# Optimization experiments

Hardware: AMD Instinct MI355X
Metric: run time of the kernel (lower is better)

Reference implementation:

```python
import jax, jax.numpy as jnp
import numpy as np

DEP_NUM, HEAD_NUM, BSZ, DIM, REL = 96, 96, 16, 512, 128


def setup_inputs() -> dict:
    key = jax.random.key(0)
    k1, k2, k3, k4 = jax.random.split(key, 4)
    outs = jax.random.normal(k1, (DEP_NUM, BSZ, DIM), dtype=jnp.float32)
    graph_state = jax.random.normal(k2, (HEAD_NUM, BSZ, DIM), dtype=jnp.float32)
    # nn.init.normal_(std=0.02) for both weights, zero biases
    Wt = 0.02 * jax.random.normal(k3, (DIM, 2 * DIM), dtype=jnp.float32)
    bt = jnp.zeros((DIM,), dtype=jnp.float32)
    Wp = 0.02 * jax.random.normal(k4, (REL, DIM), dtype=jnp.float32)
    bp = jnp.zeros((REL,), dtype=jnp.float32)
    return {"outs": outs, "graph_state": graph_state, "Wt": Wt, "bt": bt, "Wp": Wp, "bp": bp}


def reference(outs, graph_state, Wt, bt, Wp, bp):
    # outs: [dep, b, D], graph_state: [head, b, D]
    # Linear(cat(dep, head)) == dep @ Wt[:, :D].T + head @ Wt[:, D:].T + bt
    D = outs.shape[-1]
    dep_proj = jnp.einsum('dbi,ei->dbe', outs, Wt[:, :D])           # [dep, b, D]
    head_proj = jnp.einsum('hbi,ei->hbe', graph_state, Wt[:, D:])   # [head, b, D]
    # broadcast-sum to pairwise: [dep, b, head, D]
    h = jax.nn.relu(dep_proj[:, :, None, :] + jnp.swapaxes(head_proj, 0, 1)[None] + bt)
    # dropout: identity in eval mode
    scores = jnp.einsum('dbhe,re->dbhr', h, Wp) + bp                # [dep, b, head, REL]
    nil = jnp.zeros(scores.shape[:-1] + (1,), dtype=scores.dtype)
    scores = jnp.concatenate([nil, scores], axis=-1)                # [dep, b, head, REL+1]
    return jax.nn.log_softmax(scores, axis=-1)
```

## Files before the change

kernel.cpp:

```cpp
#include <hip/hip_runtime.h>
#include <math.h>

#define DEP   96
#define HEADS 96
#define BSZ   16
#define DIM   512
#define REL   128
#define RELP  129

typedef __attribute__((ext_vector_type(8))) _Float16  half8;
typedef __attribute__((ext_vector_type(2))) __fp16    fp16x2;
typedef __attribute__((ext_vector_type(4))) float     floatx4;

typedef const __attribute__((address_space(1))) unsigned int* gas_t;
typedef __attribute__((address_space(3))) unsigned int*       las_t;

__device__ __forceinline__ unsigned short f2h(float x) {
    union { _Float16 h; unsigned short u; } c;
    c.h = (_Float16)x;
    return c.u;
}
__device__ __forceinline__ unsigned pk_f2h(float a, float b) {
    union { fp16x2 h; unsigned u; } c;
    c.h = __builtin_amdgcn_cvt_pkrtz(a, b);
    return c.u;
}
__device__ __forceinline__ unsigned pk_add_h2(unsigned a, unsigned b) {
    unsigned r; asm("v_pk_add_f16 %0, %1, %2" : "=v"(r) : "v"(a), "v"(b)); return r;
}
__device__ __forceinline__ unsigned pk_max_h2(unsigned a, unsigned b) {
    unsigned r; asm("v_pk_max_f16 %0, %1, %2" : "=v"(r) : "v"(a), "v"(b)); return r;
}

#define PSS 72

__global__ __launch_bounds__(256) void proj_kernel(
    const float* __restrict__ outs, const float* __restrict__ graph,
    const float* __restrict__ Wt, const float* __restrict__ bt,
    const float* __restrict__ Wp,
    float* __restrict__ P1, unsigned short* __restrict__ P2H,
    unsigned short* __restrict__ WpH)
{
    {
        const int fb = (blockIdx.z * gridDim.y + blockIdx.y) * gridDim.x + blockIdx.x;
        if (fb < 32) {
            const int c = fb * 256 + (int)threadIdx.x;
            float4 a = *(const float4*)(Wp + (size_t)c * 8);
            float4 b = *(const float4*)(Wp + (size_t)c * 8 + 4);
            uint4 o;
            o.x = pk_f2h(a.x, a.y); o.y = pk_f2h(a.z, a.w);
            o.z = pk_f2h(b.x, b.y); o.w = pk_f2h(b.z, b.w);
            *(uint4*)(WpH + (size_t)c * 8) = o;
        }
    }

    const int z = blockIdx.z;
    const float* A = z ? graph : outs;
    const int off  = z ? DIM : 0;
    const int row0 = blockIdx.y * 64;
    const int col0 = blockIdx.x * 64;

    __shared__ __align__(16) unsigned short As[64 * PSS];
    __shared__ __align__(16) unsigned short Ws[64 * PSS];

    const int tid  = threadIdx.x;
    const int lane = tid & 63;
    const int wv   = tid >> 6;
    const int ln15 = lane & 15;
    const int quad = lane >> 4;

    floatx4 acc[4];
    #pragma unroll
    for (int nt = 0; nt < 4; ++nt) acc[nt] = (floatx4){0.f,0.f,0.f,0.f};

    for (int kt = 0; kt < DIM; kt += 64) {
        #pragma unroll
        for (int q = 0; q < 2; ++q) {
            const int slot = q*256 + tid;
            const int r  = slot >> 3;
            const int e8 = (slot & 7) * 8;
            const float* p = A + (size_t)(row0 + r) * DIM + kt + e8;
            float4 va = *(const float4*)p;
            float4 vb = *(const float4*)(p + 4);
            uint4 o;
            o.x = pk_f2h(va.x, va.y); o.y = pk_f2h(va.z, va.w);
            o.z = pk_f2h(vb.x, vb.y); o.w = pk_f2h(vb.z, vb.w);
            *(uint4*)&As[r * PSS + e8] = o;
        }
        #pragma unroll
        for (int q = 0; q < 2; ++q) {
            const int slot = q*256 + tid;
            const int r  = slot >> 3;
            const int e8 = (slot & 7) * 8;
            const float* p = Wt + (size_t)(col0 + r) * (2*DIM) + off + kt + e8;
            float4 va = *(const float4*)p;
            float4 vb = *(const float4*)(p + 4);
            uint4 o;
            o.x = pk_f2h(va.x, va.y); o.y = pk_f2h(va.z, va.w);
            o.z = pk_f2h(vb.x, vb.y); o.w = pk_f2h(vb.z, vb.w);
            *(uint4*)&Ws[r * PSS + e8] = o;
        }
        __syncthreads();
        #pragma unroll
        for (int ks = 0; ks < 64; ks += 32) {
            half8 af = *(const half8*)&As[(wv*16 + ln15) * PSS + ks + quad*8];
            #pragma unroll
            for (int nt = 0; nt < 4; ++nt) {
                half8 bf8 = *(const half8*)&Ws[(nt*16 + ln15) * PSS + ks + quad*8];
                acc[nt] = __builtin_amdgcn_mfma_f32_16x16x32_f16(af, bf8, acc[nt], 0, 0, 0);
            }
        }
        __syncthreads();
    }

    #pragma unroll
    for (int nt = 0; nt < 4; ++nt) {
        #pragma unroll
        for (int reg = 0; reg < 4; ++reg) {
            const int m = row0 + wv*16 + quad*4 + reg;
            const int n = col0 + nt*16 + ln15;
            float v = acc[nt][reg];
            if (!z) P1[(size_t)m * DIM + n] = v + bt[n];
            else    P2H[(size_t)m * DIM + n] = f2h(v);
        }
    }
}

#define HSS 72

__global__ __launch_bounds__(256, 4) void fused_kernel(
    const float* __restrict__ P1, const unsigned short* __restrict__ P2H,
    const unsigned short* __restrict__ WpH, const float* __restrict__ bp,
    float* __restrict__ out)
{
    const int db = blockIdx.x;
    const int b  = db & 15;

    __shared__ __align__(16) unsigned short drowH[DIM];
    __shared__ __align__(16) unsigned short hs[96 * HSS];
    __shared__ __align__(16) unsigned short ws[128 * 64];
    __shared__ float pmx[96][2];
    __shared__ float pl [96][2];

    const int tid  = threadIdx.x;
    const int lane = tid & 63;
    const int wv   = tid >> 6;
    const int ln15 = lane & 15;
    const int quad = lane >> 4;
    const int mh   = wv & 1;
    const int nh   = wv >> 1;
    const int e8   = (tid & 7) * 8;
    const int hb   = tid >> 3;

    const int rgrp = lane >> 3;
    const int cswz = ((lane & 7) * 16) ^ (rgrp << 4);

    {
        float2 v = *(const float2*)(P1 + (size_t)db * DIM + tid*2);
        *(unsigned*)&drowH[tid*2] = pk_f2h(v.x, v.y);
    }
    __syncthreads();

    floatx4 acc[3][4];
    #pragma unroll
    for (int i = 0; i < 3; ++i)
        #pragma unroll
        for (int j = 0; j < 4; ++j) acc[i][j] = (floatx4){0.f,0.f,0.f,0.f};

    for (int kt = 0; kt < DIM; kt += 64) {
        #pragma unroll
        for (int q = 0; q < 4; ++q) {
            const int rstart = q*32 + wv*8;
            const char* gp = (const char*)(WpH + (size_t)(rstart + rgrp) * DIM + kt) + cswz;
            __builtin_amdgcn_global_load_lds((gas_t)gp, (las_t)&ws[rstart * 64], 16, 0, 0);
        }
        uint4 dv = *(const uint4*)&drowH[kt + e8];
        #pragma unroll
        for (int q = 0; q < 3; ++q) {
            const int h = q*32 + hb;
            uint4 pv = *(const uint4*)(P2H + ((size_t)h * BSZ + b) * DIM + kt + e8);
            uint4 o;
            o.x = pk_max_h2(pk_add_h2(pv.x, dv.x), 0u);
            o.y = pk_max_h2(pk_add_h2(pv.y, dv.y), 0u);
            o.z = pk_max_h2(pk_add_h2(pv.z, dv.z), 0u);
            o.w = pk_max_h2(pk_add_h2(pv.w, dv.w), 0u);
            *(uint4*)&hs[h * HSS + e8] = o;
        }
        __syncthreads();

        #pragma unroll
        for (int ks = 0; ks < 64; ks += 32) {
            half8 af[3], bf[4];
            #pragma unroll
            for (int mt = 0; mt < 3; ++mt)
                af[mt] = *(const half8*)&hs[(mh*48 + mt*16 + ln15) * HSS + ks + quad*8];
            #pragma unroll
            for (int nt = 0; nt < 4; ++nt) {
                const int wrow = nh*64 + nt*16 + ln15;
                const int wb = wrow*128 + ((ks*2 + quad*16) ^ ((ln15 & 7) << 4));
                bf[nt] = *(const half8*)((const char*)ws + wb);
            }
            #pragma unroll
            for (int nt = 0; nt < 4; ++nt)
                #pragma unroll
                for (int mt = 0; mt < 3; ++mt)
                    acc[mt][nt] = __builtin_amdgcn_mfma_f32_16x16x32_f16(
                        af[mt], bf[nt], acc[mt][nt], 0, 0, 0);
        }
        __syncthreads();
    }

    float bpv[4];
    #pragma unroll
    for (int nt = 0; nt < 4; ++nt) bpv[nt] = bp[nh*64 + nt*16 + ln15];

    #pragma unroll
    for (int mt = 0; mt < 3; ++mt) {
        #pragma unroll
        for (int reg = 0; reg < 4; ++reg) {
            const int m = mh*48 + mt*16 + quad*4 + reg;
            float s[4];
            float mx = -1e30f;
            #pragma unroll
            for (int nt = 0; nt < 4; ++nt) {
                s[nt] = acc[mt][nt][reg] + bpv[nt];
                mx = fmaxf(mx, s[nt]);
            }
            #pragma unroll
            for (int msk = 1; msk < 16; msk <<= 1) mx = fmaxf(mx, __shfl_xor(mx, msk));
            float l = 0.f;
            #pragma unroll
            for (int nt = 0; nt < 4; ++nt) l += __expf(s[nt] - mx);
            #pragma unroll
            for (int msk = 1; msk < 16; msk <<= 1) l += __shfl_xor(l, msk);
            if (ln15 == 0) { pmx[m][nh] = mx; pl[m][nh] = l; }
        }
    }
    __syncthreads();

    #pragma unroll
    for (int mt = 0; mt < 3; ++mt) {
        #pragma unroll
        for (int reg = 0; reg < 4; ++reg) {
            const int m = mh*48 + mt*16 + quad*4 + reg;
            const float mx0 = pmx[m][0], mx1 = pmx[m][1];
            const float l0  = pl[m][0],  l1  = pl[m][1];
            const float MX = fmaxf(fmaxf(mx0, mx1), 0.f);
            const float L  = l0 * __expf(mx0 - MX) + l1 * __expf(mx1 - MX)
                           + __expf(-MX);
            const float lse = MX + __logf(L);

            const size_t base = ((size_t)db * HEADS + m) * RELP;
            #pragma unroll
            for (int nt = 0; nt < 4; ++nt)
                out[base + 1 + nh*64 + nt*16 + ln15] = acc[mt][nt][reg] + bpv[nt] - lse;
            if (nh == 0 && ln15 == 0) out[base] = -lse;
        }
    }
}

extern "C" void kernel_launch(void* const* d_in, const int* in_sizes, int n_in,
                              void* d_out, int out_size, void* d_ws, size_t ws_size,
                              hipStream_t stream) {
    const float* outs  = (const float*)d_in[0];
    const float* graph = (const float*)d_in[1];
    const float* Wt    = (const float*)d_in[2];
    const float* bt    = (const float*)d_in[3];
    const float* Wp    = (const float*)d_in[4];
    const float* bp    = (const float*)d_in[5];
    float* out = (float*)d_out;

    float* P1           = (float*)d_ws;
    unsigned short* P2H = (unsigned short*)(P1 + 786432);
    unsigned short* WpH = P2H + 786432;

    proj_kernel<<<dim3(DIM/64, (DEP*BSZ)/64, 2), 256, 0, stream>>>(
        outs, graph, Wt, bt, Wp, P1, P2H, WpH);
    fused_kernel<<<DEP*BSZ, 256, 0, stream>>>(P1, P2H, WpH, bp, out);
}
```

Before: 145.4 us.

## Stage output tile in LDS for coalesced float4 stores; load Wp via padded registers

Replaces the direct async global-to-LDS load of the Wp tile with ordinary register loads into a padded (stride 72) shared array. It also computes the log-sum-exp once per row into shared memory. The log-softmax output is then staged through a reused LDS arena in two 48-row halves and written with contiguous float4 stores. This targets the scattered, poorly coalesced scalar stores of the 129-wide output rows, at the cost of extra barriers and shared-memory round trips. Dropping the direct-to-LDS loads may add register pressure and latency.

```diff
diff --git a/kernel.cpp b/kernel.cpp
--- a/kernel.cpp
+++ b/kernel.cpp
@@ -11,9 +11,6 @@
 typedef __attribute__((ext_vector_type(8))) _Float16  half8;
 typedef __attribute__((ext_vector_type(2))) __fp16    fp16x2;
 typedef __attribute__((ext_vector_type(4))) float     floatx4;
-
-typedef const __attribute__((address_space(1))) unsigned int* gas_t;
-typedef __attribute__((address_space(3))) unsigned int*       las_t;
 
 __device__ __forceinline__ unsigned short f2h(float x) {
     union { _Float16 h; unsigned short u; } c;
@@ -127,6 +124,7 @@
 }
 
 #define HSS 72
+#define WSS 72
 
 __global__ __launch_bounds__(256, 4) void fused_kernel(
     const float* __restrict__ P1, const unsigned short* __restrict__ P2H,
@@ -136,11 +134,15 @@
     const int db = blockIdx.x;
     const int b  = db & 15;
 
+    __shared__ __align__(16) char arena[96*HSS*2 + 128*WSS*2];
+    unsigned short* hs = (unsigned short*)arena;
+    unsigned short* ws = (unsigned short*)(arena + 96*HSS*2);
+    float* outb = (float*)arena;
+
     __shared__ __align__(16) unsigned short drowH[DIM];
-    __shared__ __align__(16) unsigned short hs[96 * HSS];
-    __shared__ __align__(16) unsigned short ws[128 * 64];
     __shared__ float pmx[96][2];
     __shared__ float pl [96][2];
+    __shared__ float lseS[96];
 
     const int tid  = threadIdx.x;
     const int lane = tid & 63;
@@ -149,11 +151,6 @@
     const int quad = lane >> 4;
     const int mh   = wv & 1;
     const int nh   = wv >> 1;
-    const int e8   = (tid & 7) * 8;
-    const int hb   = tid >> 3;
-
-    const int rgrp = lane >> 3;
-    const int cswz = ((lane & 7) * 16) ^ (rgrp << 4);
 
     {
         float2 v = *(const float2*)(P1 + (size_t)db * DIM + tid*2);
@@ -169,16 +166,12 @@
 
     for (int kt = 0; kt < DIM; kt += 64) {
         #pragma unroll
-        for (int q = 0; q < 4; ++q) {
-            const int rstart = q*32 + wv*8;
-            const char* gp = (const char*)(WpH + (size_t)(rstart + rgrp) * DIM + kt) + cswz;
-            __builtin_amdgcn_global_load_lds((gas_t)gp, (las_t)&ws[rstart * 64], 16, 0, 0);
-        }
-        uint4 dv = *(const uint4*)&drowH[kt + e8];
-        #pragma unroll
         for (int q = 0; q < 3; ++q) {
-            const int h = q*32 + hb;
+            const int slot = q*256 + tid;
+            const int h  = slot >> 3;
+            const int e8 = (slot & 7) * 8;
             uint4 pv = *(const uint4*)(P2H + ((size_t)h * BSZ + b) * DIM + kt + e8);
+            uint4 dv = *(const uint4*)&drowH[kt + e8];
             uint4 o;
             o.x = pk_max_h2(pk_add_h2(pv.x, dv.x), 0u);
             o.y = pk_max_h2(pk_add_h2(pv.y, dv.y), 0u);
@@ -186,6 +179,14 @@
             o.w = pk_max_h2(pk_add_h2(pv.w, dv.w), 0u);
             *(uint4*)&hs[h * HSS + e8] = o;
         }
+        #pragma unroll
+        for (int q = 0; q < 4; ++q) {
+            const int slot = q*256 + tid;
+            const int r = slot >> 3;
+            const int g = (slot & 7) * 8;
+            *(uint4*)&ws[r * WSS + g] =
+                *(const uint4*)(WpH + (size_t)r * DIM + kt + g);
+        }
         __syncthreads();
 
         #pragma unroll
@@ -195,11 +196,8 @@
             for (int mt = 0; mt < 3; ++mt)
                 af[mt] = *(const half8*)&hs[(mh*48 + mt*16 + ln15) * HSS + ks + quad*8];
             #pragma unroll
-            for (int nt = 0; nt < 4; ++nt) {
-                const int wrow = nh*64 + nt*16 + ln15;
-                const int wb = wrow*128 + ((ks*2 + quad*16) ^ ((ln15 & 7) << 4));
-                bf[nt] = *(const half8*)((const char*)ws + wb);
-            }
+            for (int nt = 0; nt < 4; ++nt)
+                bf[nt] = *(const half8*)&ws[(nh*64 + nt*16 + ln15) * WSS + ks + quad*8];
             #pragma unroll
             for (int nt = 0; nt < 4; ++nt)
                 #pragma unroll
@@ -220,12 +218,9 @@
         for (int reg = 0; reg < 4; ++reg) {
             const int m = mh*48 + mt*16 + quad*4 + reg;
             float s[4];
-            float mx = -1e30f;
-            #pragma unroll
-            for (int nt = 0; nt < 4; ++nt) {
-                s[nt] = acc[mt][nt][reg] + bpv[nt];
-                mx = fmaxf(mx, s[nt]);
-            }
+            #pragma unroll
+            for (int nt = 0; nt < 4; ++nt) s[nt] = acc[mt][nt][reg] + bpv[nt];
+            float mx = fmaxf(fmaxf(s[0], s[1]), fmaxf(s[2], s[3]));
             #pragma unroll
             for (int msk = 1; msk < 16; msk <<= 1) mx = fmaxf(mx, __shfl_xor(mx, msk));
             float l = 0.f;
@@ -238,24 +233,38 @@
     }
     __syncthreads();
 
-    #pragma unroll
-    for (int mt = 0; mt < 3; ++mt) {
-        #pragma unroll
-        for (int reg = 0; reg < 4; ++reg) {
-            const int m = mh*48 + mt*16 + quad*4 + reg;
-            const float mx0 = pmx[m][0], mx1 = pmx[m][1];
-            const float l0  = pl[m][0],  l1  = pl[m][1];
-            const float MX = fmaxf(fmaxf(mx0, mx1), 0.f);
-            const float L  = l0 * __expf(mx0 - MX) + l1 * __expf(mx1 - MX)
-                           + __expf(-MX);
-            const float lse = MX + __logf(L);
-
-            const size_t base = ((size_t)db * HEADS + m) * RELP;
-            #pragma unroll
-            for (int nt = 0; nt < 4; ++nt)
-                out[base + 1 + nh*64 + nt*16 + ln15] = acc[mt][nt][reg] + bpv[nt] - lse;
-            if (nh == 0 && ln15 == 0) out[base] = -lse;
-        }
+    if (tid < 96) {
+        const float mx0 = pmx[tid][0], mx1 = pmx[tid][1];
+        const float MX = fmaxf(fmaxf(mx0, mx1), 0.f);
+        const float L  = pl[tid][0] * __expf(mx0 - MX) + pl[tid][1] * __expf(mx1 - MX)
+                       + __expf(-MX);
+        lseS[tid] = MX + __logf(L);
+    }
+    __syncthreads();
+
+    #pragma unroll
+    for (int g = 0; g < 2; ++g) {
+        if (mh == g) {
+            #pragma unroll
+            for (int mt = 0; mt < 3; ++mt) {
+                #pragma unroll
+                for (int reg = 0; reg < 4; ++reg) {
+                    const int lrow = mt*16 + quad*4 + reg;
+                    const float lse = lseS[g*48 + lrow];
+                    #pragma unroll
+                    for (int nt = 0; nt < 4; ++nt)
+                        outb[lrow*RELP + 1 + nh*64 + nt*16 + ln15] =
+                            acc[mt][nt][reg] + bpv[nt] - lse;
+                    if (nh == 0 && ln15 == 0) outb[lrow*RELP] = -lse;
+                }
+            }
+        }
+        __syncthreads();
+        float4* gout = (float4*)(out + (size_t)db * (HEADS*RELP) + g * (48*RELP));
+        const float4* lsrc = (const float4*)outb;
+        for (int j = tid; j < 1548; j += 256)
+            gout[j] = lsrc[j];
+        __syncthreads();
     }
 }
 
```

Measured after the change: 142.8 us. No clear change (-1.8%).
